# Kernel optimization log

Hardware: AMD Instinct MI355X
Metric: run time of the kernel (lower is better)

The kernel has to match this reference:

```python
import jax, jax.numpy as jnp
import numpy as np
import math

Z_DIM = 1024
DOWN = 512
UP = 1024
HEADS = 16
ROPE_HD = 64
HEAD_DIM = Z_DIM // HEADS  # 64, used only in softmax scale
V_HD = UP // HEADS


def _rope(x, num_heads, head_dim, base=10000.0):
    # x: [bs, L, num_heads*head_dim] -> [bs, num_heads, L, head_dim]
    bs, L, _ = x.shape
    theta = 1.0 / (base ** (jnp.arange(0, head_dim, 2, dtype=jnp.float32) / head_dim))
    pe = jnp.arange(L, dtype=jnp.float32)[:, None] * theta[None, :]  # [L, hd/2]
    # NOTE: faithful to source, which stores sin(pos) in cos_pos and cos(pos) in sin_pos
    cos_pos = jnp.repeat(jnp.sin(pe), 2, axis=-1)  # [L, hd]
    sin_pos = jnp.repeat(jnp.cos(pe), 2, axis=-1)
    q = x.reshape(bs, L, num_heads, head_dim).transpose(0, 2, 1, 3)
    q2 = jnp.stack([-q[..., 1::2], q[..., ::2]], axis=-1).reshape(q.shape)
    return q * cos_pos + q2 * sin_pos


def setup_inputs() -> dict:
    key = jax.random.key(0)
    ks = jax.random.split(key, 20)
    B, S = 2, 2048
    s = lambda fan_in: 1.0 / math.sqrt(fan_in)
    d = {
        'query': jax.random.normal(ks[0], (B, S, Z_DIM), jnp.float32),
        'key': jax.random.normal(ks[1], (B, S, Z_DIM), jnp.float32),
        'value': jax.random.normal(ks[2], (B, S, Z_DIM), jnp.float32),
        'w_dkv': jax.random.uniform(ks[3], (Z_DIM, DOWN), jnp.float32, -s(Z_DIM), s(Z_DIM)),
        'b_dkv': jnp.zeros((DOWN,), jnp.float32),
        'w_uk': jax.random.uniform(ks[4], (DOWN, UP), jnp.float32, -s(DOWN), s(DOWN)),
        'b_uk': jnp.zeros((UP,), jnp.float32),
        'w_uv': jax.random.uniform(ks[5], (DOWN, UP), jnp.float32, -s(DOWN), s(DOWN)),
        'b_uv': jnp.zeros((UP,), jnp.float32),
        'w_dq': jax.random.uniform(ks[6], (Z_DIM, DOWN), jnp.float32, -s(Z_DIM), s(Z_DIM)),
        'b_dq': jnp.zeros((DOWN,), jnp.float32),
        'w_uq': jax.random.uniform(ks[7], (DOWN, UP), jnp.float32, -s(DOWN), s(DOWN)),
        'b_uq': jnp.zeros((UP,), jnp.float32),
        'w_qr': jax.random.uniform(ks[8], (DOWN, ROPE_HD * HEADS), jnp.float32, -s(DOWN), s(DOWN)),
        'b_qr': jnp.zeros((ROPE_HD * HEADS,), jnp.float32),
        'w_kr': jax.random.uniform(ks[9], (Z_DIM, ROPE_HD), jnp.float32, -s(Z_DIM), s(Z_DIM)),
        'b_kr': jnp.zeros((ROPE_HD,), jnp.float32),
        'w_fc': jax.random.uniform(ks[10], (HEADS * V_HD, Z_DIM), jnp.float32, -s(HEADS * V_HD), s(HEADS * V_HD)),
        'b_fc': jnp.zeros((Z_DIM,), jnp.float32),
    }
    return d


def reference(query, key, value, w_dkv, b_dkv, w_uk, b_uk, w_uv, b_uv,
              w_dq, b_dq, w_uq, b_uq, w_qr, b_qr, w_kr, b_kr, w_fc, b_fc):
    bs, S, _ = query.shape
    c_t_kv = key @ w_dkv + b_dkv                      # [B,S,down]
    k_t_c = c_t_kv @ w_uk + b_uk                      # [B,S,up]
    v_t_c = c_t_kv @ w_uv + b_uv                      # [B,S,up]
    c_t_q = query @ w_dq + b_dq                       # [B,S,down]
    q_t_c = c_t_q @ w_uq + b_uq                       # [B,S,up]
    q_t_r = _rope(c_t_q @ w_qr + b_qr, HEADS, ROPE_HD)  # [B,H,S,rope_hd]
    k_t_r = _rope(key @ w_kr + b_kr, 1, ROPE_HD)         # [B,1,S,rope_hd]

    q_t_c = q_t_c.reshape(bs, S, HEADS, V_HD).transpose(0, 2, 1, 3)  # [B,H,S,dc]
    q = jnp.concatenate([q_t_c, q_t_r], axis=-1)                      # [B,H,S,dc+dr]
    k_t_c = k_t_c.reshape(bs, S, HEADS, V_HD).transpose(0, 2, 1, 3)
    k = jnp.concatenate([k_t_c, jnp.broadcast_to(k_t_r, (bs, HEADS, S, ROPE_HD))], axis=-1)

    scores = jnp.einsum('bhqd,bhkd->bhqk', q, k)
    scale = math.sqrt(HEAD_DIM) + math.sqrt(ROPE_HD)
    attn = jax.nn.softmax(scores / scale, axis=-1)    # dropout is identity (eval / p=0)

    v = v_t_c.reshape(bs, S, HEADS, V_HD).transpose(0, 2, 1, 3)
    out = jnp.einsum('bhqk,bhkd->bhqd', attn, v)      # [B,H,S,v_hd]
    out = out.transpose(0, 2, 1, 3).reshape(bs, S, HEADS * V_HD)
    return out @ w_fc + b_fc
```

## Files before the change

kernel.cpp:

```cpp
#include <hip/hip_runtime.h>
#include <hip/hip_bf16.h>
#include <hip/hip_fp16.h>

typedef __attribute__((ext_vector_type(8))) short    bf16x8;
typedef __attribute__((ext_vector_type(4))) float    f32x4;
typedef __attribute__((ext_vector_type(4))) _Float16 f16x4;
typedef __attribute__((ext_vector_type(8))) _Float16 f16x8;
typedef __attribute__((ext_vector_type(2))) __fp16   fp16x2_raw;

typedef const void __attribute__((address_space(1))) gvoid_t;
typedef void __attribute__((address_space(3)))       lvoid_t;

static __device__ __forceinline__ void gload_lds16(const void* g, void* l) {
    __builtin_amdgcn_global_load_lds((gvoid_t*)g, (lvoid_t*)l, 16, 0, 0);
}

static __device__ __forceinline__ short bfbits(float f) {
    union { __hip_bfloat16 h; short s; } u;
    u.h = __float2bfloat16(f);
    return u.s;
}

__global__ __launch_bounds__(256) void cvt_bf16_dual(const float* __restrict__ q,
                                                     const float* __restrict__ k,
                                                     __hip_bfloat16* __restrict__ qd,
                                                     __hip_bfloat16* __restrict__ kd, int n8) {
    int t = blockIdx.x * 256 + threadIdx.x;
    const float* src;
    __hip_bfloat16* dst;
    int i;
    if (t < n8)          { src = q; dst = qd; i = t; }
    else if (t < 2 * n8) { src = k; dst = kd; i = t - n8; }
    else return;
    float4 a = ((const float4*)src)[2 * i];
    float4 b = ((const float4*)src)[2 * i + 1];
    bf16x8 o;
    o[0] = bfbits(a.x); o[1] = bfbits(a.y); o[2] = bfbits(a.z); o[3] = bfbits(a.w);
    o[4] = bfbits(b.x); o[5] = bfbits(b.y); o[6] = bfbits(b.z); o[7] = bfbits(b.w);
    ((bf16x8*)dst)[i] = o;
}

struct TJob { const float* src; __hip_bfloat16* dst; int K, N, tx; };
struct TJobPack { TJob j[8]; int start[8]; };

__global__ __launch_bounds__(256) void transpose_cvt_batch(TJobPack P) {
    __shared__ __hip_bfloat16 tile[64][72];
    const int bid = blockIdx.x;
    int ji = 0;
#pragma unroll
    for (int k = 1; k < 8; ++k) if (bid >= P.start[k]) ji = k;
    const TJob J = P.j[ji];
    const int local = bid - P.start[ji];
    const int kb = (local % J.tx) * 64;
    const int nb = (local / J.tx) * 64;
    const int c  = threadIdx.x & 63;
    const int r0 = threadIdx.x >> 6;
    if (nb < J.N) {
#pragma unroll
        for (int i = 0; i < 16; ++i) {
            int r = r0 + i * 4;
            tile[r][c] = __float2bfloat16(J.src[(size_t)(kb + r) * J.N + nb + c]);
        }
        __syncthreads();
#pragma unroll
        for (int i = 0; i < 16; ++i) {
            int r = r0 + i * 4;
            J.dst[(size_t)(nb + r) * J.K + kb + c] = tile[c][r];
        }
    } else {
        __hip_bfloat16 z = __float2bfloat16(0.0f);
#pragma unroll
        for (int i = 0; i < 16; ++i) {
            int r = r0 + i * 4;
            J.dst[(size_t)(nb + r) * J.K + kb + c] = z;
        }
    }
}

__global__ __launch_bounds__(256) void bias_prep(const float* __restrict__ b_dkv, const float* __restrict__ b_kr,
                                                 const float* __restrict__ b_uk,  const float* __restrict__ b_uv,
                                                 const float* __restrict__ b_uq,  const float* __restrict__ b_qr,
                                                 float* __restrict__ bcat1, float* __restrict__ bcat2,
                                                 float* __restrict__ bcat3) {
    int t = blockIdx.x * 256 + threadIdx.x;
    if (t < 640) {
        bcat1[t] = (t < 512) ? b_dkv[t] : ((t - 512) < 64 ? b_kr[t - 512] : 0.0f);
    } else if (t < 2688) {
        int u = t - 640;
        bcat2[u] = (u < 1024) ? b_uq[u] : b_qr[u - 1024];
    } else if (t < 4736) {
        int u = t - 2688;
        bcat3[u] = (u < 1024) ? b_uk[u] : b_uv[u - 1024];
    }
}

struct GJob {
    const __hip_bfloat16* A; const __hip_bfloat16* Bt; const float* bias;
    void* C0; void* C1; int N, K, lda, ldb, ldc; float scale; int mode;
};

__global__ __launch_bounds__(256) void gemm_dual(GJob j0, GJob j1, int split) {
    __shared__ __align__(16) __hip_bfloat16 sA[2][64 * 32];
    __shared__ __align__(16) __hip_bfloat16 sB[2][128 * 32];
    const GJob J  = (blockIdx.x < (unsigned)split) ? j0 : j1;
    const int bx  = (blockIdx.x < (unsigned)split) ? blockIdx.x : blockIdx.x - split;
    const int tid  = threadIdx.x;
    const int wid  = tid >> 6;
    const int lane = tid & 63;
    const int lr   = lane & 15;
    const int lg   = lane >> 4;
    const int mb   = blockIdx.y * 64;
    const int nb   = bx * 128;
    const int wr   = (wid >> 1) * 32;
    const int wc   = (wid & 1) * 64;

    auto stage = [&](int bufi, int k0) {
        {
            int e   = wid * 512 + lane * 8;
            int row = e >> 5, col = e & 31;
            gload_lds16(J.A + (size_t)(mb + row) * J.lda + (k0 + col), &sA[bufi][wid * 512]);
        }
#pragma unroll
        for (int j = 0; j < 2; ++j) {
            int cb  = wid * 2 + j;
            int e   = cb * 512 + lane * 8;
            int row = e >> 5, col = e & 31;
            gload_lds16(J.Bt + (size_t)(nb + row) * J.ldb + (k0 + col), &sB[bufi][cb * 512]);
        }
    };

    f32x4 acc[2][4] = {};
    const int nt = J.K / 32;
    stage(0, 0);
    asm volatile("s_waitcnt vmcnt(0)" ::: "memory");
    __syncthreads();

    for (int t = 0; t < nt; ++t) {
        const int cur = t & 1;
        if (t + 1 < nt) stage(cur ^ 1, (t + 1) * 32);
        bf16x8 af[2], bfr[4];
#pragma unroll
        for (int m = 0; m < 2; ++m)
            af[m] = *(const bf16x8*)&sA[cur][(wr + m * 16 + lr) * 32 + lg * 8];
#pragma unroll
        for (int n = 0; n < 4; ++n)
            bfr[n] = *(const bf16x8*)&sB[cur][(wc + n * 16 + lr) * 32 + lg * 8];
#pragma unroll
        for (int m = 0; m < 2; ++m)
#pragma unroll
            for (int n = 0; n < 4; ++n)
                acc[m][n] = __builtin_amdgcn_mfma_f32_16x16x32_bf16(af[m], bfr[n], acc[m][n], 0, 0, 0);
        asm volatile("s_waitcnt vmcnt(0)" ::: "memory");
        __syncthreads();
    }

#pragma unroll
    for (int n = 0; n < 4; ++n) {
        int col  = nb + wc + n * 16 + lr;
        float bv = J.bias ? J.bias[col] : 0.0f;
#pragma unroll
        for (int m = 0; m < 2; ++m) {
#pragma unroll
            for (int r = 0; r < 4; ++r) {
                int row    = mb + wr + m * 16 + lg * 4 + r;
                float val  = (acc[m][n][r] + bv) * J.scale;
                if (J.mode == 1) ((float*)J.C0)[(size_t)row * J.ldc + col] = val;
                else             ((__hip_bfloat16*)J.C0)[(size_t)row * J.ldc + col] = __float2bfloat16(val);
            }
        }
    }
}

__global__ __launch_bounds__(256) void gemm128_dual(GJob j0, GJob j1, int split, int Rtot) {
    __shared__ __align__(16) char smem[128 * 132 * 2];
    __hip_bfloat16* sA = (__hip_bfloat16*)smem;
    __hip_bfloat16* sB = (__hip_bfloat16*)(smem + 16384);
    const GJob J  = (blockIdx.x < (unsigned)split) ? j0 : j1;
    const int bx  = (blockIdx.x < (unsigned)split) ? blockIdx.x : blockIdx.x - split;
    const int tid  = threadIdx.x;
    const int wid  = tid >> 6;
    const int lane = tid & 63;
    const int lr   = lane & 15;
    const int lg   = lane >> 4;
    const int mb   = blockIdx.y * 128;
    const int nb   = bx * 128;
    const int wr   = (wid >> 1) * 64;
    const int wc   = (wid & 1) * 64;

    auto stage = [&](int bufi, int k0) {
#pragma unroll
        for (int j = 0; j < 2; ++j) {
            int c   = wid * 2 + j;
            int e   = c * 512 + lane * 8;
            int row = e >> 5, col = e & 31;
            gload_lds16(J.A + (size_t)(mb + row) * J.lda + (k0 + col), &sA[bufi * 4096 + c * 512]);
        }
#pragma unroll
        for (int j = 0; j < 2; ++j) {
            int c   = wid * 2 + j;
            int e   = c * 512 + lane * 8;
            int row = e >> 5, col = e & 31;
            gload_lds16(J.Bt + (size_t)(nb + row) * J.ldb + (k0 + col), &sB[bufi * 4096 + c * 512]);
        }
    };

    f32x4 acc[4][4] = {};
    const int nt = J.K / 32;
    stage(0, 0);
    asm volatile("s_waitcnt vmcnt(0)" ::: "memory");
    __syncthreads();

    for (int t = 0; t < nt; ++t) {
        const int cur = t & 1;
        if (t + 1 < nt) stage(cur ^ 1, (t + 1) * 32);
        bf16x8 af[4], bfr[4];
#pragma unroll
        for (int m = 0; m < 4; ++m)
            af[m] = *(const bf16x8*)&sA[cur * 4096 + (wr + m * 16 + lr) * 32 + lg * 8];
#pragma unroll
        for (int n = 0; n < 4; ++n)
            bfr[n] = *(const bf16x8*)&sB[cur * 4096 + (wc + n * 16 + lr) * 32 + lg * 8];
#pragma unroll
        for (int m = 0; m < 4; ++m)
#pragma unroll
            for (int n = 0; n < 4; ++n)
                acc[m][n] = __builtin_amdgcn_mfma_f32_16x16x32_bf16(af[m], bfr[n], acc[m][n], 0, 0, 0);
        asm volatile("s_waitcnt vmcnt(0)" ::: "memory");
        __syncthreads();
    }

    if (J.mode == 3 && nb >= 1024) {
        _Float16* T = (_Float16*)smem;
#pragma unroll
        for (int n = 0; n < 4; ++n) {
            int cl = wc + n * 16 + lr;
            float bv = J.bias[nb + cl];
#pragma unroll
            for (int m = 0; m < 4; ++m)
#pragma unroll
                for (int r = 0; r < 4; ++r)
                    T[cl * 132 + wr + m * 16 + lg * 4 + r] =
                        (_Float16)((acc[m][n][r] + bv) * J.scale);
        }
        __syncthreads();
        const int vd   = tid >> 1;
        const int half = tid & 1;
        _Float16* dst = (_Float16*)J.C1 + (size_t)(nb - 1024 + vd) * Rtot + mb + half * 64;
        const _Float16* srcT = T + vd * 132 + half * 64;
#pragma unroll
        for (int j = 0; j < 8; ++j)
            *(f16x8*)&dst[j * 8] = *(const f16x8*)&srcT[j * 8];
        return;
    }

#pragma unroll
    for (int n = 0; n < 4; ++n) {
        int col  = nb + wc + n * 16 + lr;
        float bv = J.bias ? J.bias[col] : 0.0f;
#pragma unroll
        for (int m = 0; m < 4; ++m) {
#pragma unroll
            for (int r = 0; r < 4; ++r) {
                int row    = mb + wr + m * 16 + lg * 4 + r;
                float val  = (acc[m][n][r] + bv) * J.scale;
                if (J.mode == 3) ((__hip_bfloat16*)J.C0)[(size_t)row * 1024 + col] = __float2bfloat16(val);
                else             ((__hip_bfloat16*)J.C0)[(size_t)row * J.ldc + col] = __float2bfloat16(val);
            }
        }
    }
}

__global__ __launch_bounds__(256) void rope_kernel(__hip_bfloat16* __restrict__ qrope,
                                                   __hip_bfloat16* __restrict__ krope,
                                                   int R, int S) {
    int t = blockIdx.x * 256 + threadIdx.x;
    const int nq = R * 512;
    __hip_bfloat16* x;
    int i, row, rowstride, hh;
    if (t < nq)               { i = t & 31; hh = (t >> 5) & 15; row = t >> 9; x = qrope; rowstride = 2048; }
    else if (t < nq + R * 32) { t -= nq; i = t & 31; hh = 0; row = t >> 5; x = krope; rowstride = 640; }
    else return;
    int pos = row & (S - 1);
    float theta = __expf(-0.28782313662425572f * (float)i);
    float pe = (float)pos * theta;
    float sp, cp;
    __sincosf(pe, &sp, &cp);
    size_t idx = (size_t)row * rowstride + hh * 64 + 2 * i;
    float x0 = __bfloat162float(x[idx]);
    float x1 = __bfloat162float(x[idx + 1]);
    x[idx]     = __float2bfloat16(x0 * sp - x1 * cp);
    x[idx + 1] = __float2bfloat16(x1 * sp + x0 * cp);
}

__global__ __launch_bounds__(256, 2) void attn_kernel(const __hip_bfloat16* __restrict__ qcat,
                                                      const __hip_bfloat16* __restrict__ ktc,
                                                      const __hip_bfloat16* __restrict__ kr,
                                                      const _Float16* __restrict__ vtcT,
                                                      __hip_bfloat16* __restrict__ outp,
                                                      int S, int R) {
    __shared__ __align__(16) char lds[2][24 * 1024];
    const int tid  = threadIdx.x;
    const int wid  = tid >> 6;
    const int lane = tid & 63;
    const int lr   = lane & 15;
    const int lg   = lane >> 4;

    const int NQ   = S / 128;
    const int L    = blockIdx.x;
    const int slot = L >> 3;
    const int gg   = (L & 7) + 8 * (slot / NQ);
    const int qt   = slot % NQ;
    const int h    = gg & 15;
    const int b    = gg >> 4;
    const size_t base = (size_t)b * S;
    const int qb   = qt * 128 + wid * 32;

    auto stage = [&](int bufi, int kt) {
        char* bufK = lds[bufi];
        char* bufV = lds[bufi] + 16 * 1024;
#pragma unroll
        for (int j = 0; j < 4; ++j) {
            int c   = wid * 4 + j;
            int rho = c * 4 + (lane >> 4);
            int u   = (lane & 15) ^ (rho & 15);
            const __hip_bfloat16* src = (u < 8)
                ? ktc + (base + kt + rho) * 1024 + h * 64 + u * 8
                : kr  + (base + kt + rho) * 640 + (u & 7) * 8;
            gload_lds16(src, bufK + c * 1024);
        }
#pragma unroll
        for (int j = 0; j < 2; ++j) {
            int c   = wid * 2 + j;
            int rho = c * 8 + (lane >> 3);
            int u   = (lane & 7) ^ (rho & 7);
            gload_lds16(vtcT + (size_t)(h * 64 + rho) * R + base + kt + u * 8,
                        bufV + c * 1024);
        }
    };

    bf16x8 qf[2][4];
#pragma unroll
    for (int g = 0; g < 2; ++g) {
        size_t row = base + qb + g * 16 + lr;
        const __hip_bfloat16* pq = qcat + row * 2048 + h * 64;
        qf[g][0] = *(const bf16x8*)(pq + lg * 8);
        qf[g][1] = *(const bf16x8*)(pq + 32 + lg * 8);
        qf[g][2] = *(const bf16x8*)(pq + 1024 + lg * 8);
        qf[g][3] = *(const bf16x8*)(pq + 1024 + 32 + lg * 8);
    }

    f32x4 oacc[2][4] = {};
    float lrun[2] = {0.0f, 0.0f};

    const int NT = S / 64;
    stage(0, 0);
    __syncthreads();

    for (int t = 0; t < NT; ++t) {
        const int cur = t & 1;
        if (t + 1 < NT) stage(cur ^ 1, (t + 1) * 64);

        const char* bufK = lds[cur];
        const char* bufV = lds[cur] + 16 * 1024;

        f32x4 sacc[2][4] = {};
#pragma unroll
        for (int st = 0; st < 4; ++st) {
            bf16x8 kf[4];
#pragma unroll
            for (int c = 0; c < 4; ++c)
                kf[c] = *(const bf16x8*)(bufK + (st * 16 + lr) * 256 +
                                         (((c * 4 + lg) ^ lr) << 4));
#pragma unroll
            for (int g = 0; g < 2; ++g)
#pragma unroll
                for (int c = 0; c < 4; ++c)
                    sacc[g][st] = __builtin_amdgcn_mfma_f32_16x16x32_bf16(kf[c], qf[g][c], sacc[g][st], 0, 0, 0);
        }

        f16x4 vf[4][4];
#pragma unroll
        for (int st = 0; st < 4; ++st)
#pragma unroll
            for (int vt = 0; vt < 4; ++vt)
                vf[st][vt] = *(const f16x4*)(bufV + (vt * 16 + lr) * 128 +
                                             (((st * 2 + (lg >> 1)) ^ (lr & 7)) << 4) + (lg & 1) * 8);

#pragma unroll
        for (int g = 0; g < 2; ++g) {
            float p[4][4];
#pragma unroll
            for (int st = 0; st < 4; ++st)
#pragma unroll
                for (int r = 0; r < 4; ++r) {
                    p[st][r] = __builtin_exp2f(sacc[g][st][r]);
                    lrun[g] += p[st][r];
                }
#pragma unroll
            for (int st = 0; st < 4; ++st) {
                union { fp16x2_raw h2[2]; f16x4 v; } pu;
                pu.h2[0] = __builtin_amdgcn_cvt_pkrtz(p[st][0], p[st][1]);
                pu.h2[1] = __builtin_amdgcn_cvt_pkrtz(p[st][2], p[st][3]);
#pragma unroll
                for (int vt = 0; vt < 4; ++vt)
                    oacc[g][vt] = __builtin_amdgcn_mfma_f32_16x16x16f16(vf[st][vt], pu.v, oacc[g][vt], 0, 0, 0);
            }
        }
        __syncthreads();
    }

#pragma unroll
    for (int g = 0; g < 2; ++g) {
        lrun[g] += __shfl_xor(lrun[g], 16);
        lrun[g] += __shfl_xor(lrun[g], 32);
        float inv = 1.0f / lrun[g];
        size_t rowoff = (base + qb + g * 16 + lr) << 10;
#pragma unroll
        for (int vt = 0; vt < 4; ++vt)
#pragma unroll
            for (int r = 0; r < 4; ++r)
                outp[rowoff + h * 64 + vt * 16 + lg * 4 + r] =
                    __float2bfloat16(oacc[g][vt][r] * inv);
    }
}

extern "C" void kernel_launch(void* const* d_in, const int* in_sizes, int n_in,
                              void* d_out, int out_size, void* d_ws, size_t ws_size,
                              hipStream_t stream) {
    const float* query = (const float*)d_in[0];
    const float* key   = (const float*)d_in[1];
    const float* w_dkv = (const float*)d_in[3];
    const float* b_dkv = (const float*)d_in[4];
    const float* w_uk  = (const float*)d_in[5];
    const float* b_uk  = (const float*)d_in[6];
    const float* w_uv  = (const float*)d_in[7];
    const float* b_uv  = (const float*)d_in[8];
    const float* w_dq  = (const float*)d_in[9];
    const float* b_dq  = (const float*)d_in[10];
    const float* w_uq  = (const float*)d_in[11];
    const float* b_uq  = (const float*)d_in[12];
    const float* w_qr  = (const float*)d_in[13];
    const float* b_qr  = (const float*)d_in[14];
    const float* w_kr  = (const float*)d_in[15];
    const float* b_kr  = (const float*)d_in[16];
    const float* w_fc  = (const float*)d_in[17];
    const float* b_fc  = (const float*)d_in[18];

    const int B = 2;
    const int R = in_sizes[0] / 1024;
    const int S = R / B;
    const float QSCALE = 1.4426950408889634f / 16.0f;

    char* ws = (char*)d_ws;
    size_t off = 0;
    auto alloc = [&](size_t bytes) -> char* {
        char* p = ws + off;
        off += (bytes + 255) & ~(size_t)255;
        return p;
    };

    __hip_bfloat16* q_bf  = (__hip_bfloat16*)alloc((size_t)R * 1024 * 2);
    __hip_bfloat16* k_bf  = (__hip_bfloat16*)alloc((size_t)R * 1024 * 2);
    __hip_bfloat16* wcat1 = (__hip_bfloat16*)alloc(640 * 1024 * 2);
    __hip_bfloat16* wdq_t = (__hip_bfloat16*)alloc(512 * 1024 * 2);
    __hip_bfloat16* wcat3 = (__hip_bfloat16*)alloc(2048 * 512 * 2);
    __hip_bfloat16* wcat2 = (__hip_bfloat16*)alloc(2048 * 512 * 2);
    __hip_bfloat16* wfc_t = (__hip_bfloat16*)alloc(1024 * 1024 * 2);
    float*          bcat1 = (float*)alloc(640 * 4);
    float*          bcat2 = (float*)alloc(2048 * 4);
    float*          bcat3 = (float*)alloc(2048 * 4);
    __hip_bfloat16* ckkr  = (__hip_bfloat16*)alloc((size_t)R * 640 * 2);
    __hip_bfloat16* c_q   = (__hip_bfloat16*)alloc((size_t)R * 512 * 2);
    __hip_bfloat16* ktc   = (__hip_bfloat16*)alloc((size_t)R * 1024 * 2);
    _Float16*       vtcT  = (_Float16*)alloc((size_t)R * 1024 * 2);
    __hip_bfloat16* qcat  = (__hip_bfloat16*)alloc((size_t)R * 2048 * 2);
    __hip_bfloat16* attn_out = q_bf;

    cvt_bf16_dual<<<dim3(2 * R * 1024 / 8 / 256), 256, 0, stream>>>(query, key, q_bf, k_bf, R * 1024 / 8);

    TJobPack P;
    P.j[0] = {w_dkv, wcat1,              1024, 512,  16};
    P.j[1] = {w_kr,  wcat1 + 512 * 1024, 1024, 64,   16};
    P.j[2] = {w_dq,  wdq_t,              1024, 512,  16};
    P.j[3] = {w_uk,  wcat3,              512,  1024, 8};
    P.j[4] = {w_uv,  wcat3 + 1024 * 512, 512,  1024, 8};
    P.j[5] = {w_uq,  wcat2,              512,  1024, 8};
    P.j[6] = {w_qr,  wcat2 + 1024 * 512, 512,  1024, 8};
    P.j[7] = {w_fc,  wfc_t,              1024, 1024, 16};
    int st = 0;
    const int counts[8] = {128, 32, 128, 128, 128, 128, 128, 256};
    for (int i = 0; i < 8; ++i) { P.start[i] = st; st += counts[i]; }
    transpose_cvt_batch<<<dim3(st), 256, 0, stream>>>(P);

    bias_prep<<<dim3(19), 256, 0, stream>>>(b_dkv, b_kr, b_uk, b_uv, b_uq, b_qr, bcat1, bcat2, bcat3);

    GJob ja0 = {k_bf, wcat1, bcat1, ckkr, nullptr, 640, 1024, 1024, 1024, 640, 1.0f, 0};
    GJob ja1 = {q_bf, wdq_t, b_dq,  c_q,  nullptr, 512, 1024, 1024, 1024, 512, 1.0f, 0};
    gemm_dual<<<dim3(9, R / 64), 256, 0, stream>>>(ja0, ja1, 5);

    GJob jb0 = {ckkr, wcat3, bcat3, ktc,  vtcT,    2048, 512, 640, 512, 1024, 1.0f,   3};
    GJob jb1 = {c_q,  wcat2, bcat2, qcat, nullptr, 2048, 512, 512, 512, 2048, QSCALE, 0};
    gemm128_dual<<<dim3(32, R / 128), 256, 0, stream>>>(jb0, jb1, 16, R);

    rope_kernel<<<dim3((R * 512 + R * 32 + 255) / 256), 256, 0, stream>>>(qcat + 1024, ckkr + 512, R, S);

    attn_kernel<<<dim3((S / 128) * 16 * B), 256, 0, stream>>>(qcat, ktc, ckkr + 512, vtcT, attn_out, S, R);

    GJob jc0 = {attn_out, wfc_t, b_fc, d_out, nullptr, 1024, 1024, 1024, 1024, 1024, 1.0f, 1};
    gemm_dual<<<dim3(8, R / 64), 256, 0, stream>>>(jc0, jc0, 8);
}
```

Baseline: 181.0 us.

## Split attention work across 8 waves of 16 query rows each

The attention kernel now runs 512 threads per block, with each of 8 waves handling 16 query rows instead of 4 waves handling 32. This halves per-wave accumulator and fragment registers, and the staging loops are split across more waves. K and V fragments are now loaded from LDS just before each MFMA with precomputed offsets, and s_setprio raises wave priority around the MFMA sections. The aim is higher occupancy and better latency hiding. The cost is that each wave reuses K/V LDS reads over fewer query rows, so LDS read traffic per FLOP doubles.

```diff
diff --git a/kernel.cpp b/kernel.cpp
--- a/kernel.cpp
+++ b/kernel.cpp
@@ -292,7 +292,7 @@
     x[idx + 1] = __float2bfloat16(x1 * sp + x0 * cp);
 }
 
-__global__ __launch_bounds__(256, 2) void attn_kernel(const __hip_bfloat16* __restrict__ qcat,
+__global__ __launch_bounds__(512, 4) void attn_kernel(const __hip_bfloat16* __restrict__ qcat,
                                                       const __hip_bfloat16* __restrict__ ktc,
                                                       const __hip_bfloat16* __restrict__ kr,
                                                       const _Float16* __restrict__ vtcT,
@@ -313,14 +313,14 @@
     const int h    = gg & 15;
     const int b    = gg >> 4;
     const size_t base = (size_t)b * S;
-    const int qb   = qt * 128 + wid * 32;
+    const int qb   = qt * 128 + wid * 16;
 
     auto stage = [&](int bufi, int kt) {
         char* bufK = lds[bufi];
         char* bufV = lds[bufi] + 16 * 1024;
 #pragma unroll
-        for (int j = 0; j < 4; ++j) {
-            int c   = wid * 4 + j;
+        for (int j = 0; j < 2; ++j) {
+            int c   = wid * 2 + j;
             int rho = c * 4 + (lane >> 4);
             int u   = (lane & 15) ^ (rho & 15);
             const __hip_bfloat16* src = (u < 8)
@@ -328,9 +328,8 @@
                 : kr  + (base + kt + rho) * 640 + (u & 7) * 8;
             gload_lds16(src, bufK + c * 1024);
         }
-#pragma unroll
-        for (int j = 0; j < 2; ++j) {
-            int c   = wid * 2 + j;
+        {
+            int c   = wid;
             int rho = c * 8 + (lane >> 3);
             int u   = (lane & 7) ^ (rho & 7);
             gload_lds16(vtcT + (size_t)(h * 64 + rho) * R + base + kt + u * 8,
@@ -338,19 +337,26 @@
         }
     };
 
-    bf16x8 qf[2][4];
-#pragma unroll
-    for (int g = 0; g < 2; ++g) {
-        size_t row = base + qb + g * 16 + lr;
+    bf16x8 qf[4];
+    {
+        size_t row = base + qb + lr;
         const __hip_bfloat16* pq = qcat + row * 2048 + h * 64;
-        qf[g][0] = *(const bf16x8*)(pq + lg * 8);
-        qf[g][1] = *(const bf16x8*)(pq + 32 + lg * 8);
-        qf[g][2] = *(const bf16x8*)(pq + 1024 + lg * 8);
-        qf[g][3] = *(const bf16x8*)(pq + 1024 + 32 + lg * 8);
-    }
-
-    f32x4 oacc[2][4] = {};
-    float lrun[2] = {0.0f, 0.0f};
+        qf[0] = *(const bf16x8*)(pq + lg * 8);
+        qf[1] = *(const bf16x8*)(pq + 32 + lg * 8);
+        qf[2] = *(const bf16x8*)(pq + 1024 + lg * 8);
+        qf[3] = *(const bf16x8*)(pq + 1024 + 32 + lg * 8);
+    }
+
+    int kbase[4], vbase[4];
+#pragma unroll
+    for (int c = 0; c < 4; ++c)
+        kbase[c] = lr * 256 + (((c * 4 + lg) ^ lr) << 4);
+#pragma unroll
+    for (int st = 0; st < 4; ++st)
+        vbase[st] = lr * 128 + ((((st * 2 + (lg >> 1)) ^ (lr & 7)) << 4) + (lg & 1) * 8);
+
+    f32x4 oacc[4] = {};
+    float lrun = 0.0f;
 
     const int NT = S / 64;
     stage(0, 0);
@@ -363,65 +369,51 @@
         const char* bufK = lds[cur];
         const char* bufV = lds[cur] + 16 * 1024;
 
-        f32x4 sacc[2][4] = {};
+        f32x4 sacc[4] = {};
+        __builtin_amdgcn_s_setprio(1);
+#pragma unroll
+        for (int st = 0; st < 4; ++st)
+#pragma unroll
+            for (int c = 0; c < 4; ++c) {
+                bf16x8 kf = *(const bf16x8*)(bufK + st * 4096 + kbase[c]);
+                sacc[st] = __builtin_amdgcn_mfma_f32_16x16x32_bf16(kf, qf[c], sacc[st], 0, 0, 0);
+            }
+        __builtin_amdgcn_s_setprio(0);
+
+        float p[4][4];
+#pragma unroll
+        for (int st = 0; st < 4; ++st)
+#pragma unroll
+            for (int r = 0; r < 4; ++r) {
+                p[st][r] = __builtin_exp2f(sacc[st][r]);
+                lrun += p[st][r];
+            }
+        __builtin_amdgcn_s_setprio(1);
 #pragma unroll
         for (int st = 0; st < 4; ++st) {
-            bf16x8 kf[4];
-#pragma unroll
-            for (int c = 0; c < 4; ++c)
-                kf[c] = *(const bf16x8*)(bufK + (st * 16 + lr) * 256 +
-                                         (((c * 4 + lg) ^ lr) << 4));
-#pragma unroll
-            for (int g = 0; g < 2; ++g)
-#pragma unroll
-                for (int c = 0; c < 4; ++c)
-                    sacc[g][st] = __builtin_amdgcn_mfma_f32_16x16x32_bf16(kf[c], qf[g][c], sacc[g][st], 0, 0, 0);
-        }
-
-        f16x4 vf[4][4];
-#pragma unroll
-        for (int st = 0; st < 4; ++st)
-#pragma unroll
-            for (int vt = 0; vt < 4; ++vt)
-                vf[st][vt] = *(const f16x4*)(bufV + (vt * 16 + lr) * 128 +
-                                             (((st * 2 + (lg >> 1)) ^ (lr & 7)) << 4) + (lg & 1) * 8);
-
-#pragma unroll
-        for (int g = 0; g < 2; ++g) {
-            float p[4][4];
-#pragma unroll
-            for (int st = 0; st < 4; ++st)
-#pragma unroll
-                for (int r = 0; r < 4; ++r) {
-                    p[st][r] = __builtin_exp2f(sacc[g][st][r]);
-                    lrun[g] += p[st][r];
-                }
-#pragma unroll
-            for (int st = 0; st < 4; ++st) {
-                union { fp16x2_raw h2[2]; f16x4 v; } pu;
-                pu.h2[0] = __builtin_amdgcn_cvt_pkrtz(p[st][0], p[st][1]);
-                pu.h2[1] = __builtin_amdgcn_cvt_pkrtz(p[st][2], p[st][3]);
-#pragma unroll
-                for (int vt = 0; vt < 4; ++vt)
-                    oacc[g][vt] = __builtin_amdgcn_mfma_f32_16x16x16f16(vf[st][vt], pu.v, oacc[g][vt], 0, 0, 0);
+            union { fp16x2_raw h2[2]; f16x4 v; } pu;
+            pu.h2[0] = __builtin_amdgcn_cvt_pkrtz(p[st][0], p[st][1]);
+            pu.h2[1] = __builtin_amdgcn_cvt_pkrtz(p[st][2], p[st][3]);
+#pragma unroll
+            for (int vt = 0; vt < 4; ++vt) {
+                f16x4 vf = *(const f16x4*)(bufV + vt * 2048 + vbase[st]);
+                oacc[vt] = __builtin_amdgcn_mfma_f32_16x16x16f16(vf, pu.v, oacc[vt], 0, 0, 0);
             }
         }
+        __builtin_amdgcn_s_setprio(0);
         __syncthreads();
     }
 
-#pragma unroll
-    for (int g = 0; g < 2; ++g) {
-        lrun[g] += __shfl_xor(lrun[g], 16);
-        lrun[g] += __shfl_xor(lrun[g], 32);
-        float inv = 1.0f / lrun[g];
-        size_t rowoff = (base + qb + g * 16 + lr) << 10;
-#pragma unroll
-        for (int vt = 0; vt < 4; ++vt)
-#pragma unroll
-            for (int r = 0; r < 4; ++r)
-                outp[rowoff + h * 64 + vt * 16 + lg * 4 + r] =
-                    __float2bfloat16(oacc[g][vt][r] * inv);
-    }
+    lrun += __shfl_xor(lrun, 16);
+    lrun += __shfl_xor(lrun, 32);
+    float inv = 1.0f / lrun;
+    size_t rowoff = (base + qb + lr) << 10;
+#pragma unroll
+    for (int vt = 0; vt < 4; ++vt)
+#pragma unroll
+        for (int r = 0; r < 4; ++r)
+            outp[rowoff + h * 64 + vt * 16 + lg * 4 + r] =
+                __float2bfloat16(oacc[vt][r] * inv);
 }
 
 extern "C" void kernel_launch(void* const* d_in, const int* in_sizes, int n_in,
@@ -504,7 +496,7 @@
 
     rope_kernel<<<dim3((R * 512 + R * 32 + 255) / 256), 256, 0, stream>>>(qcat + 1024, ckkr + 512, R, S);
 
-    attn_kernel<<<dim3((S / 128) * 16 * B), 256, 0, stream>>>(qcat, ktc, ckkr + 512, vtcT, attn_out, S, R);
+    attn_kernel<<<dim3((S / 128) * 16 * B), 512, 0, stream>>>(qcat, ktc, ckkr + 512, vtcT, attn_out, S, R);
 
     GJob jc0 = {attn_out, wfc_t, b_fc, d_out, nullptr, 1024, 1024, 1024, 1024, 1024, 1.0f, 1};
     gemm_dual<<<dim3(8, R / 64), 256, 0, stream>>>(jc0, jc0, 8);
```

New measurement: 179.6 us. No clear change (-0.8%).
